# Performance work log

Measured on AMD Instinct MI355X. Metric: run time of the kernel, lower is better.

## Reference

```python
import jax, jax.numpy as jnp
import numpy as np

N = 100000
E = 1600000
IN_C = 128
HID = 32
HEADS = 4
NUM_CLASSES = 16
NEG_SLOPE = 0.2


def setup_inputs() -> dict:
    key = jax.random.key(0)
    ks = jax.random.split(key, 10)
    x = jax.random.normal(ks[0], (N, IN_C), dtype=jnp.float32)
    edge_index = jax.random.randint(ks[1], (2, E), 0, N, dtype=jnp.int32)
    s1 = 1.0 / np.sqrt(IN_C)
    s2 = 1.0 / np.sqrt(HID * HEADS)
    W1 = jax.random.normal(ks[2], (IN_C, HEADS * HID), dtype=jnp.float32) * s1
    att_src1 = jax.random.normal(ks[3], (HEADS, HID), dtype=jnp.float32) * s1
    att_dst1 = jax.random.normal(ks[4], (HEADS, HID), dtype=jnp.float32) * s1
    b1 = jnp.zeros((HEADS * HID,), dtype=jnp.float32)
    W2 = jax.random.normal(ks[5], (HEADS * HID, NUM_CLASSES), dtype=jnp.float32) * s2
    att_src2 = jax.random.normal(ks[6], (1, NUM_CLASSES), dtype=jnp.float32) * s2
    att_dst2 = jax.random.normal(ks[7], (1, NUM_CLASSES), dtype=jnp.float32) * s2
    b2 = jnp.zeros((NUM_CLASSES,), dtype=jnp.float32)
    return {"x": x, "edge_index": edge_index,
            "W1": W1, "att_src1": att_src1, "att_dst1": att_dst1, "b1": b1,
            "W2": W2, "att_src2": att_src2, "att_dst2": att_dst2, "b2": b2}


def _gat_conv(x, src, dst, W, att_src, att_dst, b):
    # PyG GATConv: shared linear for src/dst, additive attention, segment softmax over dst.
    n = x.shape[0]
    H, C = att_src.shape
    h = (x @ W).reshape(n, H, C)                       # [N, H, C]
    a_s = jnp.einsum('nhc,hc->nh', h, att_src)          # [N, H]
    a_d = jnp.einsum('nhc,hc->nh', h, att_dst)          # [N, H]
    e = a_s[src] + a_d[dst]                             # [E, H]
    e = jnp.where(e >= 0, e, NEG_SLOPE * e)             # leaky_relu(0.2)
    # numerically stable segment softmax over destination node groups
    e_max = jax.ops.segment_max(e, dst, num_segments=n)
    e_exp = jnp.exp(e - e_max[dst])
    denom = jax.ops.segment_sum(e_exp, dst, num_segments=n)
    alpha = e_exp / denom[dst]                          # [E, H]
    msg = h[src] * alpha[:, :, None]                    # [E, H, C]
    out = jax.ops.segment_sum(msg, dst, num_segments=n) # [N, H, C]
    return out.reshape(n, H * C) + b


def reference(x, edge_index, W1, att_src1, att_dst1, b1, W2, att_src2, att_dst2, b2):
    n = x.shape[0]
    # add_self_loops=True (PyG default), same augmented edge set for both layers
    loop = jnp.arange(n, dtype=edge_index.dtype)
    src = jnp.concatenate([edge_index[0], loop])
    dst = jnp.concatenate([edge_index[1], loop])
    h = _gat_conv(x, src, dst, W1, att_src1, att_dst1, b1)
    h = jax.nn.elu(h)
    out = _gat_conv(h, src, dst, W2, att_src2, att_dst2, b2)
    return out
```

## Files before the change

### kernel.cpp

```cpp
#include <hip/hip_runtime.h>
#include <hip/hip_bf16.h>
#include <math.h>


typedef unsigned short u16;
typedef unsigned int u32;
typedef __attribute__((ext_vector_type(8))) short bf16x8;
typedef __attribute__((ext_vector_type(4))) float f32x4;

__device__ __forceinline__ float eluf(float v) { return v > 0.f ? v : expm1f(v); }
__device__ __forceinline__ u16 f2bf(float f) {
    u32 u = __float_as_uint(f);
    u += 0x7fff + ((u >> 16) & 1);
    return (u16)(u >> 16);
}
__device__ __forceinline__ float bf2f(u16 u) {
    return __uint_as_float(((u32)u) << 16);
}
__device__ __forceinline__ float expleaky(float e) {
    float m = e >= 0.f ? 1.44269504f : 0.28853901f;
    return exp2f(e * m);
}

__global__ __launch_bounds__(256) void ksetup(
    const float* __restrict__ W1, const float* __restrict__ W2,
    const float* __restrict__ ats2, const float* __restrict__ atd2,
    u16* __restrict__ w1fh, u16* __restrict__ w1fl,
    float* __restrict__ u, float* __restrict__ v, u16* __restrict__ w2tb,
    int* __restrict__ deg, int N)
{
    const int b = blockIdx.x, tid = threadIdx.x;
    if (b < 64) {
        int idx = b * 256 + tid;
        int j = idx & 7, l = (idx >> 3) & 63, q = (idx >> 9) & 3, ct = idx >> 11;
        int k = q * 32 + (l >> 4) * 8 + j;
        int n = ct * 16 + (l & 15);
        float w = W1[k * 128 + n];
        u16 hv = f2bf(w);
        w1fh[idx] = hv;
        w1fl[idx] = f2bf(w - bf2f(hv));
    } else if (b == 64) {
        if (tid < 128) {
            float su = 0.f, sv = 0.f;
            #pragma unroll
            for (int j = 0; j < 16; ++j) {
                float w = W2[tid * 16 + j];
                su = fmaf(w, ats2[j], su);
                sv = fmaf(w, atd2[j], sv);
                w2tb[j * 128 + tid] = f2bf(w);
            }
            u[tid] = su; v[tid] = sv;
        }
    } else {
        int z = (b - 65) * 1024 + tid * 4;
        if (z < N) *(int4*)&deg[z] = make_int4(0, 0, 0, 0);
    }
}

#define REPSTRIDE 136
__global__ __launch_bounds__(256) void mega1(
    const float* __restrict__ x, const u16* __restrict__ w1fh,
    const u16* __restrict__ w1fl,
    const float* __restrict__ att_s, const float* __restrict__ att_d,
    u16* __restrict__ h1b, float* __restrict__ as1, float* __restrict__ ad1,
    int N,
    const int* __restrict__ ei, int* __restrict__ deg, int* __restrict__ rank,
    int E, int grid)
{
    __shared__ union {
        struct { u16 lh[8192]; u16 ll[8192]; } w;
        u16 rep[16384];
    } sm;
    const int tid = threadIdx.x;

    for (int e = blockIdx.x * 256 + tid; e < E; e += grid * 256) {
        int dd = ei[E + e];
        rank[e] = atomicAdd(&deg[dd], 1);
    }

    const int wv = tid >> 6, lane = tid & 63;
    const int base = blockIdx.x * 64 + wv * 16;
    const int m = lane & 15, quad = lane >> 4;

    int arow = base + m;
    if (arow >= N) arow = 0;
    const float* xr = &x[(size_t)arow * 128 + quad * 8];
    bf16x8 ah[4], al[4];
    #pragma unroll
    for (int q = 0; q < 4; ++q) {
        float4 f0 = *(const float4*)&xr[q * 32];
        float4 f1 = *(const float4*)&xr[q * 32 + 4];
        float fv[8] = {f0.x, f0.y, f0.z, f0.w, f1.x, f1.y, f1.z, f1.w};
        union { u16 us[8]; bf16x8 v; } hh, lu;
        #pragma unroll
        for (int j = 0; j < 8; ++j) {
            u16 h = f2bf(fv[j]);
            hh.us[j] = h;
            lu.us[j] = f2bf(fv[j] - bf2f(h));
        }
        ah[q] = hh.v; al[q] = lu.v;
    }

    f32x4 accs[8];
    for (int p = 0; p < 2; ++p) {
        __syncthreads();
        #pragma unroll
        for (int i = 0; i < 4; ++i) {
            int fi = (tid + i * 256) * 8;
            *(uint4*)&sm.w.lh[fi] = *(const uint4*)&w1fh[p * 8192 + fi];
            *(uint4*)&sm.w.ll[fi] = *(const uint4*)&w1fl[p * 8192 + fi];
        }
        __syncthreads();
        #pragma unroll
        for (int ctl = 0; ctl < 4; ++ctl) {
            f32x4 acc = {0.f, 0.f, 0.f, 0.f};
            #pragma unroll
            for (int q = 0; q < 4; ++q) {
                const int off = ((ctl * 4 + q) * 64 + lane) * 8;
                bf16x8 bh = *(const bf16x8*)&sm.w.lh[off];
                bf16x8 bl = *(const bf16x8*)&sm.w.ll[off];
                acc = __builtin_amdgcn_mfma_f32_16x16x32_bf16(ah[q], bh, acc, 0, 0, 0);
                acc = __builtin_amdgcn_mfma_f32_16x16x32_bf16(al[q], bh, acc, 0, 0, 0);
                acc = __builtin_amdgcn_mfma_f32_16x16x32_bf16(ah[q], bl, acc, 0, 0, 0);
            }
            accs[p * 4 + ctl] = acc;
        }
    }

    #pragma unroll
    for (int h = 0; h < 4; ++h) {
        const float cs0 = att_s[h * 32 + m];
        const float cs1 = att_s[h * 32 + 16 + m];
        const float cd0 = att_d[h * 32 + m];
        const float cd1 = att_d[h * 32 + 16 + m];
        float sp[4], dp[4];
        #pragma unroll
        for (int r = 0; r < 4; ++r) {
            sp[r] = fmaf(accs[2 * h][r], cs0, accs[2 * h + 1][r] * cs1);
            dp[r] = fmaf(accs[2 * h][r], cd0, accs[2 * h + 1][r] * cd1);
        }
        #pragma unroll
        for (int r = 0; r < 4; ++r) {
            sp[r] += __shfl_xor(sp[r], 1); sp[r] += __shfl_xor(sp[r], 2);
            sp[r] += __shfl_xor(sp[r], 4); sp[r] += __shfl_xor(sp[r], 8);
            dp[r] += __shfl_xor(dp[r], 1); dp[r] += __shfl_xor(dp[r], 2);
            dp[r] += __shfl_xor(dp[r], 4); dp[r] += __shfl_xor(dp[r], 8);
        }
        if (m == 0) {
            #pragma unroll
            for (int r = 0; r < 4; ++r) {
                int rr = base + quad * 4 + r;
                if (rr < N) {
                    as1[rr * 4 + h] = sp[r];
                    ad1[rr * 4 + h] = dp[r];
                }
            }
        }
    }

    __syncthreads();
    u16* rep = sm.rep + wv * (16 * REPSTRIDE);
    #pragma unroll
    for (int ct = 0; ct < 8; ++ct) {
        #pragma unroll
        for (int r = 0; r < 4; ++r)
            rep[(quad * 4 + r) * REPSTRIDE + ct * 16 + m] = f2bf(accs[ct][r]);
    }
    const int rr0 = lane >> 2, cc = lane & 3;
    #pragma unroll
    for (int round = 0; round < 4; ++round) {
        int chunk = cc + 4 * round;
        uint4 vv = *(const uint4*)&rep[rr0 * REPSTRIDE + chunk * 8];
        int grow = base + rr0;
        if (grow < N)
            *(uint4*)&h1b[(size_t)grow * 128 + chunk * 8] = vv;
    }
}

__global__ __launch_bounds__(256) void kscan1(
    const int* __restrict__ deg, int* __restrict__ rowptr,
    int* __restrict__ bsum, int N)
{
    __shared__ int lds[256];
    const int t = threadIdx.x;
    const int base = blockIdx.x * 1024 + t * 4;
    int v[4];
    int s = 0;
    #pragma unroll
    for (int j = 0; j < 4; ++j) {
        v[j] = (base + j < N) ? deg[base + j] : 0;
        s += v[j];
    }
    lds[t] = s;
    __syncthreads();
    for (int off = 1; off < 256; off <<= 1) {
        int y = (t >= off) ? lds[t - off] : 0;
        __syncthreads();
        lds[t] += y;
        __syncthreads();
    }
    int run = lds[t] - s;
    #pragma unroll
    for (int j = 0; j < 4; ++j) {
        if (base + j < N) rowptr[base + j] = run;
        run += v[j];
    }
    if (t == 255) bsum[blockIdx.x] = lds[255];
}

__global__ __launch_bounds__(128) void kscan2(int* __restrict__ bsum, int NB)
{
    __shared__ int lds[128];
    const int t = threadIdx.x;
    int v = (t < NB) ? bsum[t] : 0;
    lds[t] = v;
    __syncthreads();
    for (int off = 1; off < 128; off <<= 1) {
        int y = (t >= off) ? lds[t - off] : 0;
        __syncthreads();
        lds[t] += y;
        __syncthreads();
    }
    if (t < NB) bsum[t] = lds[t] - v;
}

__global__ __launch_bounds__(256) void kscat(
    const int* __restrict__ ei, const int* __restrict__ rowptr,
    const int* __restrict__ bsum, const int* __restrict__ rank,
    int* __restrict__ colidx, int E)
{
    int e = blockIdx.x * 256 + threadIdx.x;
    if (e >= E) return;
    int s = ei[e], d = ei[E + e];
    colidx[rowptr[d] + bsum[d >> 10] + rank[e]] = s;
}

__global__ __launch_bounds__(256) void kg1(
    const int* __restrict__ rowptr, const int* __restrict__ bsum,
    const int* __restrict__ colidx,
    const u16* __restrict__ h1b, const float* __restrict__ as1,
    const float* __restrict__ ad1, const float* __restrict__ b1,
    const float* __restrict__ u, const float* __restrict__ v,
    u16* __restrict__ x2b, float* __restrict__ as2, float* __restrict__ ad2,
    int N, int E)
{
    const int d = blockIdx.x * 4 + (threadIdx.x >> 6);
    if (d >= N) return;
    const int lane = threadIdx.x & 63;
    const int c = lane * 2;
    const int headB = lane >> 4;
    const int headA = lane & 3;
    const int eA = lane >> 2;

    const float adA = ad1[d * 4 + headA];
    const float wself = expleaky(as1[d * 4 + headB] + ad1[d * 4 + headB]);
    u32 hd = *(const u32*)&h1b[(d << 7) + c];
    float accx = wself * bf2f((u16)hd);
    float accy = wself * bf2f((u16)(hd >> 16));
    float den = wself;

    int i0r = rowptr[d] + bsum[d >> 10];
    int i1r = (d + 1 == N) ? E : rowptr[d + 1] + bsum[(d + 1) >> 10];
    const int i0 = __builtin_amdgcn_readfirstlane(i0r);
    const int i1 = __builtin_amdgcn_readfirstlane(i1r);

    for (int i = i0; i < i1; i += 16) {
        const int nb = min(16, i1 - i);
        const int ii = i + eA;
        const int iic = ii < i1 ? ii : i0;
        int sAv = colidx[iic];
        float wA = expleaky(as1[(sAv << 2) + headA] + adA);
        wA = (ii < i1) ? wA : 0.f;
        int e = 0;
        for (; e + 8 <= nb; e += 8) {
            int s0 = colidx[i + e + 0];
            int s1 = colidx[i + e + 1];
            int s2 = colidx[i + e + 2];
            int s3 = colidx[i + e + 3];
            int s4 = colidx[i + e + 4];
            int s5 = colidx[i + e + 5];
            int s6 = colidx[i + e + 6];
            int s7 = colidx[i + e + 7];
            float w0 = __shfl(wA, ((e + 0) << 2) + headB);
            float w1 = __shfl(wA, ((e + 1) << 2) + headB);
            float w2 = __shfl(wA, ((e + 2) << 2) + headB);
            float w3 = __shfl(wA, ((e + 3) << 2) + headB);
            float w4 = __shfl(wA, ((e + 4) << 2) + headB);
            float w5 = __shfl(wA, ((e + 5) << 2) + headB);
            float w6 = __shfl(wA, ((e + 6) << 2) + headB);
            float w7 = __shfl(wA, ((e + 7) << 2) + headB);
            u32 v0 = *(const u32*)&h1b[(s0 << 7) + c];
            u32 v1 = *(const u32*)&h1b[(s1 << 7) + c];
            u32 v2 = *(const u32*)&h1b[(s2 << 7) + c];
            u32 v3 = *(const u32*)&h1b[(s3 << 7) + c];
            u32 v4 = *(const u32*)&h1b[(s4 << 7) + c];
            u32 v5 = *(const u32*)&h1b[(s5 << 7) + c];
            u32 v6 = *(const u32*)&h1b[(s6 << 7) + c];
            u32 v7 = *(const u32*)&h1b[(s7 << 7) + c];
            accx = fmaf(w0, bf2f((u16)v0), accx); accy = fmaf(w0, bf2f((u16)(v0 >> 16)), accy);
            accx = fmaf(w1, bf2f((u16)v1), accx); accy = fmaf(w1, bf2f((u16)(v1 >> 16)), accy);
            accx = fmaf(w2, bf2f((u16)v2), accx); accy = fmaf(w2, bf2f((u16)(v2 >> 16)), accy);
            accx = fmaf(w3, bf2f((u16)v3), accx); accy = fmaf(w3, bf2f((u16)(v3 >> 16)), accy);
            accx = fmaf(w4, bf2f((u16)v4), accx); accy = fmaf(w4, bf2f((u16)(v4 >> 16)), accy);
            accx = fmaf(w5, bf2f((u16)v5), accx); accy = fmaf(w5, bf2f((u16)(v5 >> 16)), accy);
            accx = fmaf(w6, bf2f((u16)v6), accx); accy = fmaf(w6, bf2f((u16)(v6 >> 16)), accy);
            accx = fmaf(w7, bf2f((u16)v7), accx); accy = fmaf(w7, bf2f((u16)(v7 >> 16)), accy);
            den += ((w0 + w1) + (w2 + w3)) + ((w4 + w5) + (w6 + w7));
        }
        for (; e < nb; ++e) {
            int s = colidx[i + e];
            float w = __shfl(wA, (e << 2) + headB);
            u32 hv = *(const u32*)&h1b[(s << 7) + c];
            accx = fmaf(w, bf2f((u16)hv), accx);
            accy = fmaf(w, bf2f((u16)(hv >> 16)), accy);
            den += w;
        }
    }

    const float inv = 1.f / den;
    const float2 bv = *(const float2*)&b1[c];
    const float x2a = eluf(fmaf(accx, inv, bv.x));
    const float x2c = eluf(fmaf(accy, inv, bv.y));

    u32 pk = ((u32)f2bf(x2c) << 16) | (u32)f2bf(x2a);
    *(u32*)&x2b[(d << 7) + c] = pk;

    const float2 uv = *(const float2*)&u[c];
    const float2 vv = *(const float2*)&v[c];
    float sA = fmaf(x2a, uv.x, x2c * uv.y);
    float sB = fmaf(x2a, vv.x, x2c * vv.y);
    #pragma unroll
    for (int m = 1; m < 64; m <<= 1) {
        sA += __shfl_xor(sA, m);
        sB += __shfl_xor(sB, m);
    }
    if (lane == 0) { as2[d] = sA; ad2[d] = sB; }
}

__global__ __launch_bounds__(256) void kh2(
    const u16* __restrict__ x2b, const u16* __restrict__ w2tb,
    u16* __restrict__ h2b, int N)
{
    const int wv = threadIdx.x >> 6, lane = threadIdx.x & 63;
    const int n0 = blockIdx.x * 64 + wv * 16;
    if (n0 >= N) return;
    const int m = lane & 15;
    const int kq = lane >> 4;
    bf16x8 bfr[4];
    #pragma unroll
    for (int q = 0; q < 4; ++q)
        bfr[q] = *(const bf16x8*)&w2tb[m * 128 + q * 32 + kq * 8];

    int ar = n0 + m;
    if (ar >= N) ar = N - 1;
    const u16* arow = &x2b[((size_t)ar << 7) + kq * 8];
    f32x4 acc = {0.f, 0.f, 0.f, 0.f};
    #pragma unroll
    for (int q = 0; q < 4; ++q) {
        bf16x8 af = *(const bf16x8*)&arow[q * 32];
        acc = __builtin_amdgcn_mfma_f32_16x16x32_bf16(af, bfr[q], acc, 0, 0, 0);
    }
    #pragma unroll
    for (int r = 0; r < 4; ++r) {
        int rr = n0 + kq * 4 + r;
        if (rr < N) h2b[((size_t)rr << 4) + m] = f2bf(acc[r]);
    }
}

__global__ __launch_bounds__(256) void kg2(
    const int* __restrict__ rowptr, const int* __restrict__ bsum,
    const int* __restrict__ colidx,
    const u16* __restrict__ h2b, const float* __restrict__ as2,
    const float* __restrict__ ad2, const float* __restrict__ b2,
    float* __restrict__ out, int N, int E)
{
    const int d = blockIdx.x * 4 + (threadIdx.x >> 6);
    if (d >= N) return;
    const int lane = threadIdx.x & 63;
    const int ch = lane & 7, g = lane >> 3;

    const float ad_d = ad2[d];
    float acc0 = 0.f, acc1 = 0.f, den = 0.f;
    int i0r = rowptr[d] + bsum[d >> 10];
    int i1r = (d + 1 == N) ? E : rowptr[d + 1] + bsum[(d + 1) >> 10];
    const int i0 = __builtin_amdgcn_readfirstlane(i0r);
    const int i1 = __builtin_amdgcn_readfirstlane(i1r);

    for (int i = i0; i < i1; i += 64) {
        const int nb = min(64, i1 - i);
        const int idx = i + lane;
        const int idxc = idx < i1 ? idx : i0;
        int sA = colidx[idxc];
        float wA = expleaky(as2[sA] + ad_d);
        wA = (idx < i1) ? wA : 0.f;
        const int kU = (nb + 7) >> 3;
        for (int k = 0; k < kU; ++k) {
            int e = g + 8 * k;
            int ec = e < nb ? e : 0;
            float w = __shfl(wA, ec);
            int s = __shfl(sA, ec);
            if (e >= nb) w = 0.f;
            u32 hv = *(const u32*)&h2b[(s << 4) + ch * 2];
            acc0 = fmaf(w, bf2f((u16)hv), acc0);
            acc1 = fmaf(w, bf2f((u16)(hv >> 16)), acc1);
            den += w;
        }
    }
    acc0 += __shfl_xor(acc0, 8); acc0 += __shfl_xor(acc0, 16); acc0 += __shfl_xor(acc0, 32);
    acc1 += __shfl_xor(acc1, 8); acc1 += __shfl_xor(acc1, 16); acc1 += __shfl_xor(acc1, 32);
    den  += __shfl_xor(den, 8);  den  += __shfl_xor(den, 16);  den  += __shfl_xor(den, 32);

    const float wself = expleaky(as2[d] + ad_d);
    u32 hd = *(const u32*)&h2b[(d << 4) + ch * 2];
    acc0 = fmaf(wself, bf2f((u16)hd), acc0);
    acc1 = fmaf(wself, bf2f((u16)(hd >> 16)), acc1);
    den += wself;
    if (g == 0) {
        float2 ov = {acc0 / den + b2[ch * 2], acc1 / den + b2[ch * 2 + 1]};
        *(float2*)&out[(d << 4) + ch * 2] = ov;
    }
}

extern "C" void kernel_launch(void* const* d_in, const int* in_sizes, int n_in,
                              void* d_out, int out_size, void* d_ws, size_t ws_size,
                              hipStream_t stream) {
    const float* x    = (const float*)d_in[0];
    const int*   ei   = (const int*)d_in[1];
    const float* W1   = (const float*)d_in[2];
    const float* ats1 = (const float*)d_in[3];
    const float* atd1 = (const float*)d_in[4];
    const float* b1   = (const float*)d_in[5];
    const float* W2   = (const float*)d_in[6];
    const float* ats2 = (const float*)d_in[7];
    const float* atd2 = (const float*)d_in[8];
    const float* b2   = (const float*)d_in[9];
    float* out = (float*)d_out;
    const int N = in_sizes[0] / 128;
    const int E = in_sizes[1] / 2;

    u16* h1b   = (u16*)d_ws;
    u16* x2b   = h1b + (size_t)N * 128;
    u16* h2b   = x2b + (size_t)N * 128;
    u16* w2tb  = h2b + (size_t)N * 16;
    u16* w1fh  = w2tb + 2048;
    u16* w1fl  = w1fh + 16384;
    float* as1 = (float*)(w1fl + 16384);
    float* ad1 = as1 + (size_t)N * 4;
    float* as2 = ad1 + (size_t)N * 4;
    float* ad2 = as2 + N;
    float* u   = ad2 + N;
    float* v   = u + 128;
    int* deg    = (int*)(v + 128);
    int* rowptr = deg + ((N + 7) & ~3);
    int* bsum   = rowptr + ((N + 7) & ~3);
    int* colidx = bsum + 128;
    int* rank   = colidx + E;

    const int NB  = (N + 1023) / 1024;
    const int Bh1 = (N + 63) / 64;

    hipLaunchKernelGGL(ksetup, dim3(65 + NB), dim3(256), 0, stream,
                       W1, W2, ats2, atd2, w1fh, w1fl, u, v, w2tb, deg, N);
    hipLaunchKernelGGL(mega1, dim3(Bh1), dim3(256), 0, stream,
                       x, w1fh, w1fl, ats1, atd1, h1b, as1, ad1, N,
                       ei, deg, rank, E, Bh1);
    hipLaunchKernelGGL(kscan1, dim3(NB), dim3(256), 0, stream,
                       deg, rowptr, bsum, N);
    hipLaunchKernelGGL(kscan2, dim3(1), dim3(128), 0, stream, bsum, NB);
    hipLaunchKernelGGL(kscat, dim3((E + 255) / 256), dim3(256), 0, stream,
                       ei, rowptr, bsum, rank, colidx, E);
    hipLaunchKernelGGL(kg1, dim3((N + 3) / 4), dim3(256), 0, stream,
                       rowptr, bsum, colidx, h1b, as1, ad1, b1, u, v,
                       x2b, as2, ad2, N, E);
    hipLaunchKernelGGL(kh2, dim3((N + 63) / 64), dim3(256), 0, stream,
                       x2b, w2tb, h2b, N);
    hipLaunchKernelGGL(kg2, dim3((N + 3) / 4), dim3(256), 0, stream,
                       rowptr, bsum, colidx, h2b, as2, ad2, b2, out, N, E);
}
```

Measured before the change: 363.4 us.

## Make mega1 persistent with per-wave head weights held in registers

The first-layer GEMM kernel becomes a persistent grid of 1024 blocks looping over 16-row tiles. Each wave owns one attention head and keeps that head's split-bf16 W1 fragments in registers, so the per-block LDS weight staging and its barriers go away. Each tile's x rows are now loaded by all four waves instead of one, and the LDS repack buffer shrinks to a small per-wave scratch synchronised only with waitcnt. This raises x load traffic and register pressure, and the edge-degree atomic pass now runs with fewer, larger blocks.

New measurement: 372.2 us. +2.4%, slower.

```diff
diff --git a/kernel.cpp b/kernel.cpp
--- a/kernel.cpp
+++ b/kernel.cpp
@@ -57,7 +57,7 @@
     }
 }
 
-#define REPSTRIDE 136
+#define REPW 40
 __global__ __launch_bounds__(256) void mega1(
     const float* __restrict__ x, const u16* __restrict__ w1fh,
     const u16* __restrict__ w1fl,
@@ -67,77 +67,76 @@
     const int* __restrict__ ei, int* __restrict__ deg, int* __restrict__ rank,
     int E, int grid)
 {
-    __shared__ union {
-        struct { u16 lh[8192]; u16 ll[8192]; } w;
-        u16 rep[16384];
-    } sm;
+    __shared__ u16 rep[4][16 * REPW];
     const int tid = threadIdx.x;
+    const int wv = tid >> 6, lane = tid & 63;
+    const int m = lane & 15, quad = lane >> 4;
+    const int h = wv;
+
+    bf16x8 bh[2][4], bl[2][4];
+    #pragma unroll
+    for (int sub = 0; sub < 2; ++sub) {
+        #pragma unroll
+        for (int q = 0; q < 4; ++q) {
+            const int off = (((2 * h + sub) * 4 + q) * 64 + lane) * 8;
+            bh[sub][q] = *(const bf16x8*)&w1fh[off];
+            bl[sub][q] = *(const bf16x8*)&w1fl[off];
+        }
+    }
 
     for (int e = blockIdx.x * 256 + tid; e < E; e += grid * 256) {
         int dd = ei[E + e];
         rank[e] = atomicAdd(&deg[dd], 1);
     }
 
-    const int wv = tid >> 6, lane = tid & 63;
-    const int base = blockIdx.x * 64 + wv * 16;
-    const int m = lane & 15, quad = lane >> 4;
-
-    int arow = base + m;
-    if (arow >= N) arow = 0;
-    const float* xr = &x[(size_t)arow * 128 + quad * 8];
-    bf16x8 ah[4], al[4];
-    #pragma unroll
-    for (int q = 0; q < 4; ++q) {
-        float4 f0 = *(const float4*)&xr[q * 32];
-        float4 f1 = *(const float4*)&xr[q * 32 + 4];
-        float fv[8] = {f0.x, f0.y, f0.z, f0.w, f1.x, f1.y, f1.z, f1.w};
-        union { u16 us[8]; bf16x8 v; } hh, lu;
-        #pragma unroll
-        for (int j = 0; j < 8; ++j) {
-            u16 h = f2bf(fv[j]);
-            hh.us[j] = h;
-            lu.us[j] = f2bf(fv[j] - bf2f(h));
-        }
-        ah[q] = hh.v; al[q] = lu.v;
-    }
-
-    f32x4 accs[8];
-    for (int p = 0; p < 2; ++p) {
-        __syncthreads();
-        #pragma unroll
-        for (int i = 0; i < 4; ++i) {
-            int fi = (tid + i * 256) * 8;
-            *(uint4*)&sm.w.lh[fi] = *(const uint4*)&w1fh[p * 8192 + fi];
-            *(uint4*)&sm.w.ll[fi] = *(const uint4*)&w1fl[p * 8192 + fi];
-        }
-        __syncthreads();
-        #pragma unroll
-        for (int ctl = 0; ctl < 4; ++ctl) {
-            f32x4 acc = {0.f, 0.f, 0.f, 0.f};
+    const float cs0 = att_s[h * 32 + m];
+    const float cs1 = att_s[h * 32 + 16 + m];
+    const float cd0 = att_d[h * 32 + m];
+    const float cd1 = att_d[h * 32 + 16 + m];
+
+    u16* myrep = rep[wv];
+    const int ntile = (N + 15) >> 4;
+
+    for (int t = blockIdx.x; t < ntile; t += grid) {
+        const int r0 = t << 4;
+        int arow = r0 + m;
+        if (arow >= N) arow = N - 1;
+        const float* xr = &x[(size_t)arow * 128 + quad * 8];
+
+        bf16x8 ah[4], al[4];
+        #pragma unroll
+        for (int q = 0; q < 4; ++q) {
+            float4 f0 = *(const float4*)&xr[q * 32];
+            float4 f1 = *(const float4*)&xr[q * 32 + 4];
+            float fv[8] = {f0.x, f0.y, f0.z, f0.w, f1.x, f1.y, f1.z, f1.w};
+            union { u16 us[8]; bf16x8 v; } hh, lu;
+            #pragma unroll
+            for (int j = 0; j < 8; ++j) {
+                u16 hvv = f2bf(fv[j]);
+                hh.us[j] = hvv;
+                lu.us[j] = f2bf(fv[j] - bf2f(hvv));
+            }
+            ah[q] = hh.v; al[q] = lu.v;
+        }
+
+        f32x4 acc[2];
+        #pragma unroll
+        for (int sub = 0; sub < 2; ++sub) {
+            f32x4 a = {0.f, 0.f, 0.f, 0.f};
             #pragma unroll
             for (int q = 0; q < 4; ++q) {
-                const int off = ((ctl * 4 + q) * 64 + lane) * 8;
-                bf16x8 bh = *(const bf16x8*)&sm.w.lh[off];
-                bf16x8 bl = *(const bf16x8*)&sm.w.ll[off];
-                acc = __builtin_amdgcn_mfma_f32_16x16x32_bf16(ah[q], bh, acc, 0, 0, 0);
-                acc = __builtin_amdgcn_mfma_f32_16x16x32_bf16(al[q], bh, acc, 0, 0, 0);
-                acc = __builtin_amdgcn_mfma_f32_16x16x32_bf16(ah[q], bl, acc, 0, 0, 0);
+                a = __builtin_amdgcn_mfma_f32_16x16x32_bf16(ah[q], bh[sub][q], a, 0, 0, 0);
+                a = __builtin_amdgcn_mfma_f32_16x16x32_bf16(al[q], bh[sub][q], a, 0, 0, 0);
+                a = __builtin_amdgcn_mfma_f32_16x16x32_bf16(ah[q], bl[sub][q], a, 0, 0, 0);
             }
-            accs[p * 4 + ctl] = acc;
-        }
-    }
-
-    #pragma unroll
-    for (int h = 0; h < 4; ++h) {
-        const float cs0 = att_s[h * 32 + m];
-        const float cs1 = att_s[h * 32 + 16 + m];
-        const float cd0 = att_d[h * 32 + m];
-        const float cd1 = att_d[h * 32 + 16 + m];
+            acc[sub] = a;
+        }
+
         float sp[4], dp[4];
         #pragma unroll
         for (int r = 0; r < 4; ++r) {
-            sp[r] = fmaf(accs[2 * h][r], cs0, accs[2 * h + 1][r] * cs1);
-            dp[r] = fmaf(accs[2 * h][r], cd0, accs[2 * h + 1][r] * cd1);
+            sp[r] = fmaf(acc[0][r], cs0, acc[1][r] * cs1);
+            dp[r] = fmaf(acc[0][r], cd0, acc[1][r] * cd1);
         }
         #pragma unroll
         for (int r = 0; r < 4; ++r) {
@@ -149,31 +148,27 @@
         if (m == 0) {
             #pragma unroll
             for (int r = 0; r < 4; ++r) {
-                int rr = base + quad * 4 + r;
+                int rr = r0 + quad * 4 + r;
                 if (rr < N) {
                     as1[rr * 4 + h] = sp[r];
                     ad1[rr * 4 + h] = dp[r];
                 }
             }
         }
-    }
-
-    __syncthreads();
-    u16* rep = sm.rep + wv * (16 * REPSTRIDE);
-    #pragma unroll
-    for (int ct = 0; ct < 8; ++ct) {
-        #pragma unroll
-        for (int r = 0; r < 4; ++r)
-            rep[(quad * 4 + r) * REPSTRIDE + ct * 16 + m] = f2bf(accs[ct][r]);
-    }
-    const int rr0 = lane >> 2, cc = lane & 3;
-    #pragma unroll
-    for (int round = 0; round < 4; ++round) {
-        int chunk = cc + 4 * round;
-        uint4 vv = *(const uint4*)&rep[rr0 * REPSTRIDE + chunk * 8];
-        int grow = base + rr0;
+
+        #pragma unroll
+        for (int sub = 0; sub < 2; ++sub) {
+            #pragma unroll
+            for (int r = 0; r < 4; ++r)
+                myrep[(quad * 4 + r) * REPW + sub * 16 + m] = f2bf(acc[sub][r]);
+        }
+        __asm__ __volatile__("s_waitcnt lgkmcnt(0)" ::: "memory");
+        __builtin_amdgcn_sched_barrier(0);
+        const int rr = lane >> 2, cc = lane & 3;
+        uint4 vv = *(const uint4*)&myrep[rr * REPW + cc * 8];
+        const int grow = r0 + rr;
         if (grow < N)
-            *(uint4*)&h1b[(size_t)grow * 128 + chunk * 8] = vv;
+            *(uint4*)&h1b[(size_t)grow * 128 + h * 32 + cc * 8] = vv;
     }
 }
 
@@ -456,14 +451,14 @@
     int* colidx = bsum + 128;
     int* rank   = colidx + E;
 
-    const int NB  = (N + 1023) / 1024;
-    const int Bh1 = (N + 63) / 64;
+    const int NB = (N + 1023) / 1024;
+    const int G1 = 1024;
 
     hipLaunchKernelGGL(ksetup, dim3(65 + NB), dim3(256), 0, stream,
                        W1, W2, ats2, atd2, w1fh, w1fl, u, v, w2tb, deg, N);
-    hipLaunchKernelGGL(mega1, dim3(Bh1), dim3(256), 0, stream,
+    hipLaunchKernelGGL(mega1, dim3(G1), dim3(256), 0, stream,
                        x, w1fh, w1fl, ats1, atd1, h1b, as1, ad1, N,
-                       ei, deg, rank, E, Bh1);
+                       ei, deg, rank, E, G1);
     hipLaunchKernelGGL(kscan1, dim3(NB), dim3(256), 0, stream,
                        deg, rowptr, bsum, N);
     hipLaunchKernelGGL(kscan2, dim3(1), dim3(128), 0, stream, bsum, NB);
```
